# Kernel optimization log

Hardware: AMD Instinct MI355X
Metric: run time of the kernel (lower is better)

Reference implementation:

```python
import jax, jax.numpy as jnp
import numpy as np

C_IN, C_OUT, K, PAD, STRIDE = 128, 256, 3, 1, 1
H = W = 256


def setup_inputs() -> dict:
    key = jax.random.key(0)
    k1, k2, k3 = jax.random.split(key, 3)
    # batch=1: the original forward uses X_pad[0] for every batch index,
    # so with m=1 the buggy loop and a standard conv are mathematically identical.
    x = jax.random.normal(k1, (1, C_IN, H, W), dtype=jnp.float32)
    # nn.Parameter(torch.rand(...)) -> uniform[0,1)
    weight = jax.random.uniform(k2, (C_OUT, C_IN, K, K), dtype=jnp.float32)
    bias = jax.random.uniform(k3, (C_OUT,), dtype=jnp.float32)
    return {"x": x, "weight": weight, "bias": bias}


def reference(x, weight, bias):
    # Faithful math of convAppx.forward with FP_appx_mul treated as exact
    # multiply (FP_appx_mul is not defined in the source): a plain 2D
    # cross-correlation (no kernel flip, matching the sliced elementwise
    # product) with symmetric padding, stride 1, plus per-channel bias.
    z = jax.lax.conv_general_dilated(
        x, weight,
        window_strides=(STRIDE, STRIDE),
        padding=((PAD, PAD), (PAD, PAD)),
        dimension_numbers=("NCHW", "OIHW", "NCHW"),
    )
    return z + bias[None, :, None, None]
```

## Files before the change

kernel.cpp:

```cpp
#include <hip/hip_runtime.h>
#include <hip/hip_bf16.h>


typedef short bf16x8 __attribute__((ext_vector_type(8)));
typedef float f32x4 __attribute__((ext_vector_type(4)));
typedef unsigned short u16x4 __attribute__((ext_vector_type(4)));
typedef unsigned short u16x8 __attribute__((ext_vector_type(8)));

#define CIN   128
#define COUT  256
#define HH    256
#define WW    256
#define HP    258
#define ROWP  (HP * CIN)

static __device__ __forceinline__ unsigned short f2bf(float v) {
    __hip_bfloat16 b = __float2bfloat16(v);
    return *reinterpret_cast<unsigned short*>(&b);
}

static __device__ __forceinline__ void gload_lds16(const unsigned short* g, unsigned short* l) {
    __builtin_amdgcn_global_load_lds(
        (const __attribute__((address_space(1))) unsigned int*)g,
        (__attribute__((address_space(3))) unsigned int*)l, 16, 0, 0);
}

__global__ __launch_bounds__(256) void prep_kernel(const float* __restrict__ x,
                                                   const float* __restrict__ w,
                                                   unsigned short* __restrict__ xb,
                                                   unsigned short* __restrict__ wr) {
    int bid = blockIdx.x;
    int t   = threadIdx.x;

    if (bid < 65) {
        int i = bid * 256 + t;
        if (i < 16448) {
            u16x8 z = {0, 0, 0, 0, 0, 0, 0, 0};
            int off;
            if (i < 8256) {
                int r   = (i >= 4128) ? 1 : 0;
                int rem = i - r * 4128;
                off = (r * 257) * ROWP + rem * 8;
            } else {
                int j   = i - 8256;
                int col = j >> 12;
                int rem = j & 4095;
                int hp  = (rem >> 4) + 1;
                int c8  = rem & 15;
                off = hp * ROWP + (col * 257) * CIN + c8 * 8;
            }
            *(u16x8*)(&xb[off]) = z;
        }
    }

    if (bid < 128) {
        int p = bid * 256 + t;
        const float* src = w + p * 9;
        #pragma unroll
        for (int khw = 0; khw < 9; ++khw)
            wr[khw * (COUT * CIN) + p] = f2bf(src[khw]);
    }

    int h  = bid >> 2;
    int w0 = (bid & 3) * 64;
    __shared__ unsigned short tile[CIN * 72];

    int wq  = t & 15;
    int cib = t >> 4;
    for (int c0 = 0; c0 < CIN; c0 += 16) {
        int ci = c0 + cib;
        float4 v = *(const float4*)(x + ci * (HH * WW) + h * WW + w0 + wq * 4);
        u16x4 p;
        p.x = f2bf(v.x); p.y = f2bf(v.y); p.z = f2bf(v.z); p.w = f2bf(v.w);
        *(u16x4*)(&tile[ci * 72 + wq * 4]) = p;
    }
    __syncthreads();

    for (int it = 0; it < 4; ++it) {
        int idx = it * 256 + t;
        int ww_ = idx & 63;
        int c8  = idx >> 6;
        u16x8 o;
        #pragma unroll
        for (int j = 0; j < 8; ++j)
            o[j] = tile[(c8 * 8 + j) * 72 + ww_];
        int dst = ((h + 1) * HP + (w0 + ww_ + 1)) * CIN + c8 * 8;
        *(u16x8*)(&xb[dst]) = o;
    }
}

__global__ __launch_bounds__(256) void conv_mfma_kernel(const unsigned short* __restrict__ xb,
                                                        const unsigned short* __restrict__ wr,
                                                        const float* __restrict__ bias,
                                                        float* __restrict__ out) {
    __shared__ unsigned short As[128 * 64];
    __shared__ unsigned short Bs[128 * 64];

    int bid  = blockIdx.x;
    int co_t = bid & 1;
    int wh   = (bid >> 1) & 1;
    int h    = bid >> 2;
    int co0  = co_t * 128;
    int p0   = h * WW + wh * 128;

    int t    = threadIdx.x;
    int wave = t >> 6;
    int lane = t & 63;
    int wm   = wave >> 1;
    int wn   = wave & 1;
    int quad = lane >> 4;
    int l16  = lane & 15;
    int sw   = l16 & 7;

    int lr = lane >> 3;
    int s  = lane & 7;
    int cs = (s ^ lr) * 8;

    f32x4 acc[4][4];
    #pragma unroll
    for (int mi = 0; mi < 4; ++mi)
        #pragma unroll
        for (int ni = 0; ni < 4; ++ni)
            acc[mi][ni] = (f32x4){0.f, 0.f, 0.f, 0.f};

    for (int kh = 0; kh < 3; ++kh) {
        for (int kw = 0; kw < 3; ++kw) {
            int khw = kh * 3 + kw;
            const unsigned short* xsrc = xb + (size_t)((h + kh) * HP + wh * 128 + kw) * CIN;
            const unsigned short* wsrc = wr + (size_t)khw * (COUT * CIN) + co0 * CIN;
            for (int cc = 0; cc < 2; ++cc) {
                int kofs = cc * 64;
                __syncthreads();
                #pragma unroll
                for (int it = 0; it < 4; ++it) {
                    int cid = wave * 4 + it;
                    int r   = cid * 8 + lr;
                    int ge  = kofs + cs;
                    gload_lds16(wsrc + r * CIN + ge, &As[cid * 512]);
                    gload_lds16(xsrc + r * CIN + ge, &Bs[cid * 512]);
                }
                __syncthreads();
                #pragma unroll
                for (int kk = 0; kk < 2; ++kk) {
                    bf16x8 af[4], bfr[4];
                    #pragma unroll
                    for (int mi = 0; mi < 4; ++mi) {
                        int row = wm * 64 + mi * 16 + l16;
                        af[mi] = *(bf16x8*)(&As[row * 64 + ((kk * 4 + quad) ^ sw) * 8]);
                    }
                    #pragma unroll
                    for (int ni = 0; ni < 4; ++ni) {
                        int row = wn * 64 + ni * 16 + l16;
                        bfr[ni] = *(bf16x8*)(&Bs[row * 64 + ((kk * 4 + quad) ^ sw) * 8]);
                    }
                    #pragma unroll
                    for (int mi = 0; mi < 4; ++mi)
                        #pragma unroll
                        for (int ni = 0; ni < 4; ++ni)
                            acc[mi][ni] = __builtin_amdgcn_mfma_f32_16x16x32_bf16(
                                af[mi], bfr[ni], acc[mi][ni], 0, 0, 0);
                }
            }
        }
    }

    #pragma unroll
    for (int mi = 0; mi < 4; ++mi) {
        #pragma unroll
        for (int r = 0; r < 4; ++r) {
            int co = co0 + wm * 64 + mi * 16 + quad * 4 + r;
            float b = bias[co];
            float* orow = out + (size_t)co * (HH * WW) + p0 + wn * 64 + l16;
            #pragma unroll
            for (int ni = 0; ni < 4; ++ni)
                orow[ni * 16] = acc[mi][ni][r] + b;
        }
    }
}

extern "C" void kernel_launch(void* const* d_in, const int* in_sizes, int n_in,
                              void* d_out, int out_size, void* d_ws, size_t ws_size,
                              hipStream_t stream) {
    const float* x    = (const float*)d_in[0];
    const float* w    = (const float*)d_in[1];
    const float* bias = (const float*)d_in[2];
    float* out        = (float*)d_out;

    unsigned short* xb = (unsigned short*)d_ws;
    unsigned short* wr = xb + (size_t)HP * HP * CIN;

    prep_kernel<<<dim3(1024), dim3(256), 0, stream>>>(x, w, xb, wr);
    conv_mfma_kernel<<<dim3(1024), dim3(256), 0, stream>>>(xb, wr, bias, out);
}
```

Measured before the change: 137.9 us.

## Reuse input row tile across kw taps and load full channel depth per stage

```diff
diff --git a/kernel.cpp b/kernel.cpp
--- a/kernel.cpp
+++ b/kernel.cpp
@@ -93,8 +93,8 @@
                                                         const unsigned short* __restrict__ wr,
                                                         const float* __restrict__ bias,
                                                         float* __restrict__ out) {
-    __shared__ unsigned short As[128 * 64];
-    __shared__ unsigned short Bs[128 * 64];
+    __shared__ unsigned short Bw[130 * 128];
+    __shared__ unsigned short As[128 * 128];
 
     int bid  = blockIdx.x;
     int co_t = bid & 1;
@@ -110,11 +110,6 @@
     int wn   = wave & 1;
     int quad = lane >> 4;
     int l16  = lane & 15;
-    int sw   = l16 & 7;
-
-    int lr = lane >> 3;
-    int s  = lane & 7;
-    int cs = (s ^ lr) * 8;
 
     f32x4 acc[4][4];
     #pragma unroll
@@ -126,40 +121,57 @@
     for (int kh = 0; kh < 3; ++kh) {
         for (int kw = 0; kw < 3; ++kw) {
             int khw = kh * 3 + kw;
-            const unsigned short* xsrc = xb + (size_t)((h + kh) * HP + wh * 128 + kw) * CIN;
-            const unsigned short* wsrc = wr + (size_t)khw * (COUT * CIN) + co0 * CIN;
-            for (int cc = 0; cc < 2; ++cc) {
-                int kofs = cc * 64;
-                __syncthreads();
-                #pragma unroll
-                for (int it = 0; it < 4; ++it) {
-                    int cid = wave * 4 + it;
-                    int r   = cid * 8 + lr;
-                    int ge  = kofs + cs;
-                    gload_lds16(wsrc + r * CIN + ge, &As[cid * 512]);
-                    gload_lds16(xsrc + r * CIN + ge, &Bs[cid * 512]);
-                }
-                __syncthreads();
-                #pragma unroll
-                for (int kk = 0; kk < 2; ++kk) {
-                    bf16x8 af[4], bfr[4];
+            __syncthreads();
+            if (kw == 0) {
+                const unsigned short* xrow = xb + (size_t)((h + kh) * HP + wh * 128) * CIN;
+                #pragma unroll
+                for (int it = 0; it < 8; ++it) {
+                    int seg = it * 256 + t;
+                    int col = seg >> 4;
+                    int s   = seg & 15;
+                    int c   = s ^ (col & 15);
+                    gload_lds16(xrow + col * CIN + c * 8, &Bw[seg * 8]);
+                }
+                if (t < 32) {
+                    int seg = 2048 + t;
+                    int col = seg >> 4;
+                    int s   = seg & 15;
+                    int c   = s ^ (col & 15);
+                    gload_lds16(xrow + col * CIN + c * 8, &Bw[seg * 8]);
+                }
+            }
+            {
+                const unsigned short* wsrc = wr + (size_t)khw * (COUT * CIN) + co0 * CIN;
+                #pragma unroll
+                for (int it = 0; it < 8; ++it) {
+                    int seg = it * 256 + t;
+                    int r   = seg >> 4;
+                    int s   = seg & 15;
+                    int c   = s ^ (r & 15);
+                    gload_lds16(wsrc + r * CIN + c * 8, &As[seg * 8]);
+                }
+            }
+            __syncthreads();
+            #pragma unroll
+            for (int kk = 0; kk < 4; ++kk) {
+                int chunk = kk * 4 + quad;
+                bf16x8 af[4], bfr[4];
+                #pragma unroll
+                for (int mi = 0; mi < 4; ++mi) {
+                    int row = wm * 64 + mi * 16 + l16;
+                    af[mi] = *(bf16x8*)(&As[row * 128 + (chunk ^ l16) * 8]);
+                }
+                #pragma unroll
+                for (int ni = 0; ni < 4; ++ni) {
+                    int col = wn * 64 + ni * 16 + l16 + kw;
+                    bfr[ni] = *(bf16x8*)(&Bw[col * 128 + (chunk ^ (col & 15)) * 8]);
+                }
+                #pragma unroll
+                for (int mi = 0; mi < 4; ++mi)
                     #pragma unroll
-                    for (int mi = 0; mi < 4; ++mi) {
-                        int row = wm * 64 + mi * 16 + l16;
-                        af[mi] = *(bf16x8*)(&As[row * 64 + ((kk * 4 + quad) ^ sw) * 8]);
-                    }
-                    #pragma unroll
-                    for (int ni = 0; ni < 4; ++ni) {
-                        int row = wn * 64 + ni * 16 + l16;
-                        bfr[ni] = *(bf16x8*)(&Bs[row * 64 + ((kk * 4 + quad) ^ sw) * 8]);
-                    }
-                    #pragma unroll
-                    for (int mi = 0; mi < 4; ++mi)
-                        #pragma unroll
-                        for (int ni = 0; ni < 4; ++ni)
-                            acc[mi][ni] = __builtin_amdgcn_mfma_f32_16x16x32_bf16(
-                                af[mi], bfr[ni], acc[mi][ni], 0, 0, 0);
-                }
+                    for (int ni = 0; ni < 4; ++ni)
+                        acc[mi][ni] = __builtin_amdgcn_mfma_f32_16x16x32_bf16(
+                            af[mi], bfr[ni], acc[mi][ni], 0, 0, 0);
             }
         }
     }
```

Measured after the change: 135.9 us. About the same (-1.5%).
